# Kernel optimization log

Measured on AMD Instinct MI355X. Metric: run time of the kernel, lower is better.

Reference implementation:

```python
import jax, jax.numpy as jnp
import numpy as np

# Model / shape constants (match init_kwargs and input_specs)
E, H, N, B = 1024, 16, 4096, 4
D = E // H               # head_dim = 64
W_SZ, EXT, C_SZ = 128, 128, 128   # window, ext window, rf chunk
NEG = -1e9


def _linear(x, w, b):
    # torch nn.Linear convention: w is (out, in)
    return x @ w.T + b


def _layernorm(x, g, b, eps=1e-5):
    m = jnp.mean(x, -1, keepdims=True)
    v = jnp.mean((x - m) ** 2, -1, keepdims=True)
    return (x - m) * jax.lax.rsqrt(v + eps) * g + b


def _ext_windows(x, w, ext):
    # x: (b,h,n,d) -> (b,h,g,ext+w,d); window g covers keys [g*w-ext, g*w+w)
    # (front-padded with zeros, same as causal_window_1d_partition + as_strided)
    g = x.shape[2] // w
    xp = jnp.pad(x, ((0, 0), (0, 0), (ext, 0), (0, 0)))
    idx = jnp.arange(g)[:, None] * w + jnp.arange(ext + w)[None, :]
    return xp[:, :, idx]


def setup_inputs() -> dict:
    key = jax.random.key(0)
    ks = jax.random.split(key, 20)
    p = lambda i, shape: jax.random.normal(ks[i], shape, jnp.float32) * 0.02
    return {
        'query': jax.random.normal(ks[0], (N, B, E), jnp.float32),
        'Wq': p(1, (E, E)), 'bq': jnp.zeros((E,), jnp.float32),
        'Wk': p(2, (E, E)), 'bk': jnp.zeros((E,), jnp.float32),
        'Wv': p(3, (E, E)), 'bv': jnp.zeros((E,), jnp.float32),
        'Wo': p(4, (E, E)), 'bo': jnp.zeros((E,), jnp.float32),
        'mu_q_w': p(5, (D, D)), 'mu_q_b': jnp.zeros((D,), jnp.float32),
        'mu_q_g': jnp.ones((D,), jnp.float32), 'mu_q_be': jnp.zeros((D,), jnp.float32),
        'mu_k_w': p(6, (D, D)), 'mu_k_b': jnp.zeros((D,), jnp.float32),
        'mu_k_g': jnp.ones((D,), jnp.float32), 'mu_k_be': jnp.zeros((D,), jnp.float32),
    }


def reference(query, Wq, bq, Wk, bk, Wv, bv, Wo, bo,
              mu_q_w, mu_q_b, mu_q_g, mu_q_be,
              mu_k_w, mu_k_b, mu_k_g, mu_k_be):
    n, b, e = query.shape
    h, d = H, D
    scaling = d ** -0.5

    q = _linear(query, Wq, bq)
    k = _linear(query, Wk, bk)
    v = _linear(query, Wv, bv)
    to_bhnd = lambda t: jnp.transpose(t.reshape(n, b, h, d), (1, 2, 0, 3))
    q, k, v = to_bhnd(q), to_bhnd(k), to_bhnd(v)
    q = q * scaling

    # ---------------- local causal windowed attention scores ----------------
    g = n // W_SZ
    w_q = q.reshape(b, h, g, W_SZ, d)
    w_k = _ext_windows(k, W_SZ, EXT)   # (b,h,g,EXT+W,d)
    w_v = _ext_windows(v, W_SZ, EXT)
    local_dots = jnp.einsum('bhgid,bhgjd->bhgij', w_q, w_k)
    i = jnp.arange(W_SZ)[:, None]
    j = jnp.arange(EXT + W_SZ)[None, :]
    causal_ok = j <= i + EXT                      # key pos <= query pos
    gi = jnp.arange(g)[:, None, None]
    valid = j[None] >= (EXT - gi * W_SZ)          # mask zero-padded front keys
    local_mask = causal_ok[None] & valid          # (g, W, EXT+W)
    local_dots = jnp.where(local_mask[None, None], local_dots, NEG)

    # ------------- random-feature (EVA) chunk-level global branch -------------
    nc = n // C_SZ
    rf_q = q.reshape(b, h, nc, C_SZ, d)
    rf_k = k.reshape(b, h, nc, C_SZ, d)
    rf_v = v.reshape(b, h, nc, C_SZ, d)
    rf_q_bar = _layernorm(_linear(rf_q.mean(-2), mu_q_w, mu_q_b), mu_q_g, mu_q_be)
    rf_k_bar = _layernorm(_linear(rf_k.mean(-2), mu_k_w, mu_k_b), mu_k_g, mu_k_be)
    mu = rf_q_bar + rf_k_bar   # eval mode: weights = mu (no Gaussian noise)

    # prm_projection(rf_k, mu) with normalize=False, then softmax within chunk
    norm = scaling * jnp.sum(rf_k ** 2, -1) / 2.0            # (b,h,nc,p)
    log_proj_k = jnp.einsum('bhcd,bhcpd->bhcp', mu, rf_k) * scaling - norm
    beta = jax.nn.softmax(log_proj_k, -1)
    rfa_chunk = jnp.einsum('bhcp,bhcpd->bhcd', beta, rf_v)   # SNIS chunk values

    rfa_dots = jnp.einsum('bhgid,bhcd->bhgic', w_q, rf_k_bar)
    # chunk c visible to window g iff the whole chunk precedes the window
    chunk_vis = (jnp.arange(nc)[None, :] + 1) * C_SZ <= jnp.arange(g)[:, None] * W_SZ
    rfa_dots = jnp.where(chunk_vis[None, None, :, None, :], rfa_dots, NEG)

    # joint softmax over [local keys | global chunk pseudo-keys]
    attn = jax.nn.softmax(jnp.concatenate([local_dots, rfa_dots], -1), -1)
    la, ga = attn[..., : EXT + W_SZ], attn[..., EXT + W_SZ:]
    out = jnp.einsum('bhgij,bhgjd->bhgid', la, w_v) \
        + jnp.einsum('bhgic,bhcd->bhgid', ga, rfa_chunk)

    out = out.reshape(b, h, n, d)
    out = jnp.transpose(out, (2, 0, 1, 3)).reshape(n, b, e)
    return _linear(out, Wo, bo)
```

## Files before the change

kernel.cpp:

```cpp
#include <hip/hip_runtime.h>
#include <hip/hip_bf16.h>

typedef __hip_bfloat16 bf16;
typedef __attribute__((ext_vector_type(8))) short bf16x8;
typedef __attribute__((ext_vector_type(4))) float f32x4;

#define E_DIM 1024
#define H_DIM 16
#define N_DIM 4096
#define B_DIM 4
#define D_DIM 64
#define G_WIN 32
#define NC 32
#define M_ROWS 16384

__global__ __launch_bounds__(256) void cvt_f32_bf16(
    const float* __restrict__ in, bf16* __restrict__ out)
{
    int i = (blockIdx.x * 256 + threadIdx.x) * 8;
    float4 f0 = *(const float4*)(in + i);
    float4 f1 = *(const float4*)(in + i + 4);
    union { bf16 t[8]; uint4 u; } pk;
    pk.t[0] = (bf16)f0.x; pk.t[1] = (bf16)f0.y; pk.t[2] = (bf16)f0.z; pk.t[3] = (bf16)f0.w;
    pk.t[4] = (bf16)f1.x; pk.t[5] = (bf16)f1.y; pk.t[6] = (bf16)f1.z; pk.t[7] = (bf16)f1.w;
    *(uint4*)(out + i) = pk.u;
}

template<int MODE, bool WB16>
__global__ __launch_bounds__(256) void gemm_mfma(
    const bf16* __restrict__ A, const void* __restrict__ Wp,
    const float* __restrict__ bias, float scale,
    bf16* __restrict__ out_bf, float* __restrict__ out_f)
{
    __shared__ bf16 As[128 * 32];
    __shared__ bf16 Bs[128 * 32];
    int tid  = threadIdx.x;
    int lane = tid & 63;
    int wv   = tid >> 6;
    int wm   = (wv >> 1) * 64;
    int wn   = (wv & 1) * 64;
    int quad = lane >> 4;
    int l16  = lane & 15;

    int nwg = gridDim.x;
    int per = nwg >> 3;
    int logical = (blockIdx.x & 7) * per + (blockIdx.x >> 3);
    int col0 = (logical & 7) * 128;
    int row0 = (logical >> 3) * 128;

    f32x4 acc[4][4] = {};

    for (int k0 = 0; k0 < E_DIM; k0 += 32) {
#pragma unroll
        for (int i = 0; i < 2; i++) {
            int idx = tid + i * 256;
            int r = idx >> 2, c = idx & 3;
            const bf16* g = A + (size_t)(row0 + r) * E_DIM + k0 + c * 8;
            __builtin_amdgcn_global_load_lds(
                (const __attribute__((address_space(1))) void*)g,
                (__attribute__((address_space(3))) void*)(As + idx * 8), 16, 0, 0);
        }
        if constexpr (WB16) {
            const bf16* Wb = (const bf16*)Wp;
#pragma unroll
            for (int i = 0; i < 2; i++) {
                int idx = tid + i * 256;
                int e = idx >> 2, c = idx & 3;
                const bf16* g = Wb + (size_t)(col0 + e) * E_DIM + k0 + c * 8;
                __builtin_amdgcn_global_load_lds(
                    (const __attribute__((address_space(1))) void*)g,
                    (__attribute__((address_space(3))) void*)(Bs + idx * 8), 16, 0, 0);
            }
        } else {
            const float* Wf = (const float*)Wp;
#pragma unroll
            for (int i = 0; i < 2; i++) {
                int idx = tid + i * 256;
                int e = idx >> 2, c = idx & 3;
                const float* wr = Wf + (size_t)(col0 + e) * E_DIM + k0 + c * 8;
                float4 f0 = *(const float4*)wr;
                float4 f1 = *(const float4*)(wr + 4);
                union { bf16 t[8]; uint4 u; } pk;
                pk.t[0] = (bf16)f0.x; pk.t[1] = (bf16)f0.y;
                pk.t[2] = (bf16)f0.z; pk.t[3] = (bf16)f0.w;
                pk.t[4] = (bf16)f1.x; pk.t[5] = (bf16)f1.y;
                pk.t[6] = (bf16)f1.z; pk.t[7] = (bf16)f1.w;
                *(uint4*)(Bs + idx * 8) = pk.u;
            }
        }
        __syncthreads();

        bf16x8 af[4], bfr[4];
#pragma unroll
        for (int t = 0; t < 4; t++) {
            af[t]  = *(const bf16x8*)(As + (wm + t * 16 + l16) * 32 + quad * 8);
            bfr[t] = *(const bf16x8*)(Bs + (wn + t * 16 + l16) * 32 + quad * 8);
        }
#pragma unroll
        for (int mt = 0; mt < 4; mt++)
#pragma unroll
            for (int nt = 0; nt < 4; nt++)
                acc[mt][nt] = __builtin_amdgcn_mfma_f32_16x16x32_bf16(
                    af[mt], bfr[nt], acc[mt][nt], 0, 0, 0);
        __syncthreads();
    }

#pragma unroll
    for (int mt = 0; mt < 4; mt++)
#pragma unroll
        for (int nt = 0; nt < 4; nt++)
#pragma unroll
            for (int rg = 0; rg < 4; rg++) {
                int m = row0 + wm + mt * 16 + quad * 4 + rg;
                int e = col0 + wn + nt * 16 + l16;
                float val = acc[mt][nt][rg];
                if (MODE == 0) {
                    float v2 = (val + bias[e]) * scale;
                    int n = m >> 2, bb = m & 3;
                    int h = e >> 6, d = e & 63;
                    out_bf[((((size_t)bb * H_DIM + h) * N_DIM + n) * D_DIM) + d] = (bf16)v2;
                } else {
                    out_f[(size_t)m * E_DIM + e] = val + bias[e];
                }
            }
}

__global__ __launch_bounds__(128) void chunk_stats(
    const bf16* __restrict__ q_s, const bf16* __restrict__ kbuf, const bf16* __restrict__ vbuf,
    const float* __restrict__ mqw, const float* __restrict__ mqb,
    const float* __restrict__ mqg, const float* __restrict__ mqbe,
    const float* __restrict__ mkw, const float* __restrict__ mkb,
    const float* __restrict__ mkg, const float* __restrict__ mkbe,
    float* __restrict__ rf_k_bar, float* __restrict__ rfa_chunk)
{
    int bid = blockIdx.x;
    int c = bid % NC;
    int bh = bid / NC;
    int tid = threadIdx.x;

    __shared__ float qm[64], km[64], qb_s[64], kb_s[64], mu_s[64], sc[128];
    __shared__ float stats[4];

    size_t base = ((size_t)bh * N_DIM + c * 128) * D_DIM;

    if (tid < 64) {
        float s = 0.f;
        for (int p = 0; p < 128; p++) s += (float)q_s[base + p * 64 + tid];
        qm[tid] = s * (1.0f / 128.0f);
    } else {
        int d = tid - 64;
        float s = 0.f;
        for (int p = 0; p < 128; p++) s += (float)kbuf[base + p * 64 + d];
        km[d] = s * (1.0f / 128.0f);
    }
    __syncthreads();

    if (tid < 64) {
        float t = mqb[tid];
        for (int d2 = 0; d2 < 64; d2++) t += qm[d2] * mqw[tid * 64 + d2];
        qb_s[tid] = t;
    } else {
        int d = tid - 64;
        float t = mkb[d];
        for (int d2 = 0; d2 < 64; d2++) t += km[d2] * mkw[d * 64 + d2];
        kb_s[d] = t;
    }
    __syncthreads();

    if (tid == 0) {
        float m = 0.f;
        for (int d = 0; d < 64; d++) m += qb_s[d];
        m *= (1.0f / 64.0f);
        float vv = 0.f;
        for (int d = 0; d < 64; d++) { float x = qb_s[d] - m; vv += x * x; }
        vv *= (1.0f / 64.0f);
        stats[0] = m; stats[1] = rsqrtf(vv + 1e-5f);
    } else if (tid == 64) {
        float m = 0.f;
        for (int d = 0; d < 64; d++) m += kb_s[d];
        m *= (1.0f / 64.0f);
        float vv = 0.f;
        for (int d = 0; d < 64; d++) { float x = kb_s[d] - m; vv += x * x; }
        vv *= (1.0f / 64.0f);
        stats[2] = m; stats[3] = rsqrtf(vv + 1e-5f);
    }
    __syncthreads();

    if (tid < 64) {
        float qn = (qb_s[tid] - stats[0]) * stats[1] * mqg[tid] + mqbe[tid];
        float kn = (kb_s[tid] - stats[2]) * stats[3] * mkg[tid] + mkbe[tid];
        mu_s[tid] = qn + kn;
        rf_k_bar[(size_t)bh * NC * 64 + c * 64 + tid] = kn;
    }
    __syncthreads();

    {
        float dot = 0.f, ss = 0.f;
        const bf16* kr = kbuf + base + tid * 64;
        for (int d = 0; d < 64; d++) {
            float kv = (float)kr[d];
            dot += mu_s[d] * kv;
            ss += kv * kv;
        }
        sc[tid] = dot * 0.125f - 0.125f * 0.5f * ss;
    }
    __syncthreads();
    if (tid == 0) {
        float m = sc[0];
        for (int p = 1; p < 128; p++) m = fmaxf(m, sc[p]);
        stats[0] = m;
    }
    __syncthreads();
    float e = expf(sc[tid] - stats[0]);
    sc[tid] = e;
    __syncthreads();
    if (tid == 0) {
        float s = 0.f;
        for (int p = 0; p < 128; p++) s += sc[p];
        stats[1] = 1.0f / s;
    }
    __syncthreads();
    sc[tid] *= stats[1];
    __syncthreads();

    if (tid < 64) {
        float acc = 0.f;
        for (int p = 0; p < 128; p++) acc += sc[p] * (float)vbuf[base + p * 64 + tid];
        rfa_chunk[(size_t)bh * NC * 64 + c * 64 + tid] = acc;
    }
}

__global__ __launch_bounds__(512, 4) void attn_kernel(
    const bf16* __restrict__ qin, const bf16* __restrict__ kbuf, const bf16* __restrict__ vbuf,
    const float* __restrict__ rf_k_bar, const float* __restrict__ rfa_chunk,
    bf16* __restrict__ aout)
{
    int bid = blockIdx.x;
    int g = bid & (G_WIN - 1);
    int bh = bid / G_WIN;
    int b = bh >> 4, h = bh & 15;
    int tid = threadIdx.x;
    int lane = tid & 63;
    int wv = tid >> 6;
    int q4 = lane >> 4;
    int l16 = lane & 15;

    __shared__ __align__(16) short Ks[288 * 72];
    __shared__ __align__(16) short Vt[64 * 296];

    size_t kvbase = (size_t)bh * N_DIM * D_DIM;
    int k0g = g * 128 - 128;

#pragma unroll
    for (int i = 0; i < 4; i++) {
        int ci = tid + i * 512;
        int key = ci >> 3, chc = ci & 7;
        int kidx = k0g + key; if (kidx < 0) kidx = 0;
        bf16x8 v = *(const bf16x8*)(kbuf + kvbase + (size_t)kidx * 64 + chc * 8);
        *(bf16x8*)(Ks + key * 72 + chc * 8) = v;
    }
    if (tid < 256) {
        int c = tid >> 3, chc = tid & 7;
        const float* src = rf_k_bar + (size_t)bh * NC * 64 + c * 64 + chc * 8;
        float4 f0 = *(const float4*)src;
        float4 f1 = *(const float4*)(src + 4);
        union { bf16 t[8]; bf16x8 v; } pk;
        pk.t[0] = (bf16)f0.x; pk.t[1] = (bf16)f0.y;
        pk.t[2] = (bf16)f0.z; pk.t[3] = (bf16)f0.w;
        pk.t[4] = (bf16)f1.x; pk.t[5] = (bf16)f1.y;
        pk.t[6] = (bf16)f1.z; pk.t[7] = (bf16)f1.w;
        *(bf16x8*)(Ks + (256 + c) * 72 + chc * 8) = pk.v;
    }
#pragma unroll
    for (int i = 0; i < 4; i++) {
        int ci = tid + i * 512;
        int key = ci & 255, dc = ci >> 8;
        int kidx = k0g + key; if (kidx < 0) kidx = 0;
        union { bf16x8 v; short s[8]; } u;
        u.v = *(const bf16x8*)(vbuf + kvbase + (size_t)kidx * 64 + dc * 8);
#pragma unroll
        for (int jj = 0; jj < 8; jj++)
            Vt[(dc * 8 + jj) * 296 + key] = u.s[jj];
    }
    if (tid < 256) {
        int d = tid >> 2, cg = tid & 3;
        const float* rc = rfa_chunk + (size_t)bh * NC * 64;
#pragma unroll
        for (int jj = 0; jj < 8; jj++) {
            int c = cg * 8 + jj;
            union { bf16 bv; short s; } cv;
            cv.bv = (bf16)rc[(size_t)c * 64 + d];
            Vt[d * 296 + 256 + c] = cv.s;
        }
    }

    bf16x8 aq[2];
    {
        const bf16* qrow = qin + kvbase + (size_t)(g * 128 + wv * 16 + l16) * 64 + q4 * 8;
        aq[0] = *(const bf16x8*)qrow;
        aq[1] = *(const bf16x8*)(qrow + 32);
    }

    __syncthreads();

    f32x4 acc[18] = {};
#pragma unroll
    for (int ct = 0; ct < 18; ct++) {
#pragma unroll
        for (int kc = 0; kc < 2; kc++) {
            bf16x8 bk = *(const bf16x8*)(Ks + (ct * 16 + l16) * 72 + kc * 32 + q4 * 8);
            acc[ct] = __builtin_amdgcn_mfma_f32_16x16x32_bf16(aq[kc], bk, acc[ct], 0, 0, 0);
        }
    }

    __syncthreads();

    float mrow[4] = { -1e30f, -1e30f, -1e30f, -1e30f };
#pragma unroll
    for (int ct = 0; ct < 18; ct++) {
        int j = ct * 16 + l16;
        bool jval = (j < 256) ? (k0g + j >= 0) : ((j - 256) < g);
#pragma unroll
        for (int rg = 0; rg < 4; rg++) {
            int i = wv * 16 + q4 * 4 + rg;
            bool ok = jval && (j >= 256 || j <= i + 128);
            float s = ok ? acc[ct][rg] : -1e9f;
            acc[ct][rg] = s;
            mrow[rg] = fmaxf(mrow[rg], s);
        }
    }
#pragma unroll
    for (int rg = 0; rg < 4; rg++) {
        float v = mrow[rg];
        v = fmaxf(v, __shfl_xor(v, 1));
        v = fmaxf(v, __shfl_xor(v, 2));
        v = fmaxf(v, __shfl_xor(v, 4));
        v = fmaxf(v, __shfl_xor(v, 8));
        mrow[rg] = v;
    }

    float rsum[4] = { 0.f, 0.f, 0.f, 0.f };
#pragma unroll
    for (int ct = 0; ct < 18; ct++)
#pragma unroll
        for (int rg = 0; rg < 4; rg++) {
            float p = __expf(acc[ct][rg] - mrow[rg]);
            acc[ct][rg] = p;
            rsum[rg] += p;
        }
    float rinv[4];
#pragma unroll
    for (int rg = 0; rg < 4; rg++) {
        float v = rsum[rg];
        v += __shfl_xor(v, 1);
        v += __shfl_xor(v, 2);
        v += __shfl_xor(v, 4);
        v += __shfl_xor(v, 8);
        rinv[rg] = 1.0f / v;
    }

    f32x4 accO[4] = {};
    short* pw = Ks + wv * (16 * 40);
#pragma unroll
    for (int cc = 0; cc < 9; cc++) {
#pragma unroll
        for (int half = 0; half < 2; half++) {
            int ct = cc * 2 + half;
#pragma unroll
            for (int rg = 0; rg < 4; rg++) {
                union { bf16 bv; short s; } cv;
                cv.bv = (bf16)acc[ct][rg];
                pw[(q4 * 4 + rg) * 40 + half * 16 + l16] = cv.s;
            }
        }
        bf16x8 ap = *(const bf16x8*)(pw + l16 * 40 + q4 * 8);
#pragma unroll
        for (int dt = 0; dt < 4; dt++) {
            bf16x8 bv = *(const bf16x8*)(Vt + (dt * 16 + l16) * 296 + cc * 32 + q4 * 8);
            accO[dt] = __builtin_amdgcn_mfma_f32_16x16x32_bf16(ap, bv, accO[dt], 0, 0, 0);
        }
    }

    int nbase = g * 128 + wv * 16 + q4 * 4;
#pragma unroll
    for (int dt = 0; dt < 4; dt++)
#pragma unroll
        for (int rg = 0; rg < 4; rg++) {
            float o = accO[dt][rg] * rinv[rg];
            int nn = nbase + rg;
            int d = dt * 16 + l16;
            aout[((size_t)nn * B_DIM + b) * E_DIM + h * 64 + d] = (bf16)o;
        }
}

extern "C" void kernel_launch(void* const* d_in, const int* in_sizes, int n_in,
                              void* d_out, int out_size, void* d_ws, size_t ws_size,
                              hipStream_t stream) {
    const float* query = (const float*)d_in[0];
    const float* Wq   = (const float*)d_in[1];
    const float* bq   = (const float*)d_in[2];
    const float* Wk   = (const float*)d_in[3];
    const float* bk   = (const float*)d_in[4];
    const float* Wv   = (const float*)d_in[5];
    const float* bv   = (const float*)d_in[6];
    const float* Wo   = (const float*)d_in[7];
    const float* bo   = (const float*)d_in[8];
    const float* mqw  = (const float*)d_in[9];
    const float* mqb  = (const float*)d_in[10];
    const float* mqg  = (const float*)d_in[11];
    const float* mqbe = (const float*)d_in[12];
    const float* mkw  = (const float*)d_in[13];
    const float* mkb  = (const float*)d_in[14];
    const float* mkg  = (const float*)d_in[15];
    const float* mkbe = (const float*)d_in[16];

    const size_t SZ = (size_t)B_DIM * H_DIM * N_DIM * D_DIM;
    const size_t STATS = (size_t)B_DIM * H_DIM * NC * D_DIM;

    bf16* kb = (bf16*)d_ws;
    bf16* vb = kb + SZ;
    float* rf_k_bar  = (float*)(vb + SZ);
    float* rfa_chunk = rf_k_bar + STATS;

    size_t base_bytes = 2 * SZ * sizeof(bf16) + 2 * STATS * sizeof(float);
    size_t wmat = (size_t)E_DIM * E_DIM;
    bool wb16   = ws_size >= base_bytes + 4 * wmat * sizeof(bf16);
    bool big_ws = ws_size >= base_bytes + 4 * wmat * sizeof(bf16) + SZ * sizeof(bf16);
    bf16* wq_b = (bf16*)((char*)d_ws + base_bytes);
    bf16* wk_b = wq_b + wmat;
    bf16* wv_b = wk_b + wmat;
    bf16* wo_b = wv_b + wmat;
    bf16* att_ws = wo_b + wmat;

    float* outf = (float*)d_out;
    bf16* qb  = (bf16*)d_out;
    bf16* qbf = qb + SZ;

    dim3 gblk(256);
    int ggrd = (E_DIM / 128) * (M_ROWS / 128);

    cvt_f32_bf16<<<(M_ROWS * E_DIM) / (256 * 8), 256, 0, stream>>>(query, qbf);
    if (wb16) {
        int wblk = (int)(wmat / (256 * 8));
        cvt_f32_bf16<<<wblk, 256, 0, stream>>>(Wq, wq_b);
        cvt_f32_bf16<<<wblk, 256, 0, stream>>>(Wk, wk_b);
        cvt_f32_bf16<<<wblk, 256, 0, stream>>>(Wv, wv_b);
        cvt_f32_bf16<<<wblk, 256, 0, stream>>>(Wo, wo_b);
    }

    if (wb16) {
        gemm_mfma<0, true><<<ggrd, gblk, 0, stream>>>(qbf, wq_b, bq, 0.125f, qb, nullptr);
        gemm_mfma<0, true><<<ggrd, gblk, 0, stream>>>(qbf, wk_b, bk, 1.0f, kb, nullptr);
        gemm_mfma<0, true><<<ggrd, gblk, 0, stream>>>(qbf, wv_b, bv, 1.0f, vb, nullptr);
    } else {
        gemm_mfma<0, false><<<ggrd, gblk, 0, stream>>>(qbf, Wq, bq, 0.125f, qb, nullptr);
        gemm_mfma<0, false><<<ggrd, gblk, 0, stream>>>(qbf, Wk, bk, 1.0f, kb, nullptr);
        gemm_mfma<0, false><<<ggrd, gblk, 0, stream>>>(qbf, Wv, bv, 1.0f, vb, nullptr);
    }

    chunk_stats<<<B_DIM * H_DIM * NC, 128, 0, stream>>>(
        qb, kb, vb, mqw, mqb, mqg, mqbe, mkw, mkb, mkg, mkbe, rf_k_bar, rfa_chunk);

    bf16* attn_dst = big_ws ? att_ws : qbf;
    attn_kernel<<<B_DIM * H_DIM * G_WIN, 512, 0, stream>>>(
        qb, kb, vb, rf_k_bar, rfa_chunk, attn_dst);

    const bf16* gemm_in;
    if (big_ws) {
        gemm_in = att_ws;
    } else {
        (void)hipMemcpyAsync(kb, qbf, SZ * sizeof(bf16), hipMemcpyDeviceToDevice, stream);
        gemm_in = kb;
    }

    if (wb16) {
        gemm_mfma<1, true><<<ggrd, gblk, 0, stream>>>(gemm_in, wo_b, bo, 1.0f, nullptr, outf);
    } else {
        gemm_mfma<1, false><<<ggrd, gblk, 0, stream>>>(gemm_in, Wo, bo, 1.0f, nullptr, outf);
    }
}
```

Before: 432.9 us.

## Compute transposed scores in attention so P stays in registers for PV MFMA

Swaps the MFMA operand order in the windowed attention kernel so each lane holds the scores for one query row. Rows are then reduced with two cross-lane shuffles instead of per-row 4-step shuffles. V columns are stored in a permuted key order so the bf16 probabilities can be packed straight from the accumulators as the PV operand, removing the LDS round trip for P and one __syncthreads. Output is written as packed 4-element stores. The permuted layout must match the MFMA register mapping exactly, or the results will be wrong.

```diff
diff --git a/kernel.cpp b/kernel.cpp
--- a/kernel.cpp
+++ b/kernel.cpp
@@ -13,6 +13,9 @@
 #define G_WIN 32
 #define NC 32
 #define M_ROWS 16384
+
+#define AS1 __attribute__((address_space(1)))
+#define AS3 __attribute__((address_space(3)))
 
 __global__ __launch_bounds__(256) void cvt_f32_bf16(
     const float* __restrict__ in, bf16* __restrict__ out)
@@ -57,8 +60,7 @@
             int r = idx >> 2, c = idx & 3;
             const bf16* g = A + (size_t)(row0 + r) * E_DIM + k0 + c * 8;
             __builtin_amdgcn_global_load_lds(
-                (const __attribute__((address_space(1))) void*)g,
-                (__attribute__((address_space(3))) void*)(As + idx * 8), 16, 0, 0);
+                (const AS1 void*)g, (AS3 void*)(As + idx * 8), 16, 0, 0);
         }
         if constexpr (WB16) {
             const bf16* Wb = (const bf16*)Wp;
@@ -68,8 +70,7 @@
                 int e = idx >> 2, c = idx & 3;
                 const bf16* g = Wb + (size_t)(col0 + e) * E_DIM + k0 + c * 8;
                 __builtin_amdgcn_global_load_lds(
-                    (const __attribute__((address_space(1))) void*)g,
-                    (__attribute__((address_space(3))) void*)(Bs + idx * 8), 16, 0, 0);
+                    (const AS1 void*)g, (AS3 void*)(Bs + idx * 8), 16, 0, 0);
             }
         } else {
             const float* Wf = (const float*)Wp;
@@ -278,9 +279,11 @@
         int kidx = k0g + key; if (kidx < 0) kidx = 0;
         union { bf16x8 v; short s[8]; } u;
         u.v = *(const bf16x8*)(vbuf + kvbase + (size_t)kidx * 64 + dc * 8);
+        int colp = (key & ~31) | (((key >> 2) & 3) << 3)
+                 | (((key >> 4) & 1) << 2) | (key & 3);
 #pragma unroll
         for (int jj = 0; jj < 8; jj++)
-            Vt[(dc * 8 + jj) * 296 + key] = u.s[jj];
+            Vt[(dc * 8 + jj) * 296 + colp] = u.s[jj];
     }
     if (tid < 256) {
         int d = tid >> 2, cg = tid & 3;
@@ -288,17 +291,18 @@
 #pragma unroll
         for (int jj = 0; jj < 8; jj++) {
             int c = cg * 8 + jj;
+            int p = (((c >> 2) & 3) << 3) | (((c >> 4) & 1) << 2) | (c & 3);
             union { bf16 bv; short s; } cv;
             cv.bv = (bf16)rc[(size_t)c * 64 + d];
-            Vt[d * 296 + 256 + c] = cv.s;
-        }
-    }
-
-    bf16x8 aq[2];
+            Vt[d * 296 + 256 + p] = cv.s;
+        }
+    }
+
+    bf16x8 bq0, bq1;
     {
         const bf16* qrow = qin + kvbase + (size_t)(g * 128 + wv * 16 + l16) * 64 + q4 * 8;
-        aq[0] = *(const bf16x8*)qrow;
-        aq[1] = *(const bf16x8*)(qrow + 32);
+        bq0 = *(const bf16x8*)qrow;
+        bq1 = *(const bf16x8*)(qrow + 32);
     }
 
     __syncthreads();
@@ -306,91 +310,68 @@
     f32x4 acc[18] = {};
 #pragma unroll
     for (int ct = 0; ct < 18; ct++) {
-#pragma unroll
-        for (int kc = 0; kc < 2; kc++) {
-            bf16x8 bk = *(const bf16x8*)(Ks + (ct * 16 + l16) * 72 + kc * 32 + q4 * 8);
-            acc[ct] = __builtin_amdgcn_mfma_f32_16x16x32_bf16(aq[kc], bk, acc[ct], 0, 0, 0);
-        }
-    }
-
-    __syncthreads();
-
-    float mrow[4] = { -1e30f, -1e30f, -1e30f, -1e30f };
+        int r = ct * 16 + l16;
+        bf16x8 ak0 = *(const bf16x8*)(Ks + r * 72 + q4 * 8);
+        bf16x8 ak1 = *(const bf16x8*)(Ks + r * 72 + 32 + q4 * 8);
+        acc[ct] = __builtin_amdgcn_mfma_f32_16x16x32_bf16(ak0, bq0, acc[ct], 0, 0, 0);
+        acc[ct] = __builtin_amdgcn_mfma_f32_16x16x32_bf16(ak1, bq1, acc[ct], 0, 0, 0);
+    }
+
+    int qi = wv * 16 + l16;
+    float m = -1e30f;
 #pragma unroll
     for (int ct = 0; ct < 18; ct++) {
-        int j = ct * 16 + l16;
-        bool jval = (j < 256) ? (k0g + j >= 0) : ((j - 256) < g);
+        int jbase = ct * 16 + q4 * 4;
 #pragma unroll
         for (int rg = 0; rg < 4; rg++) {
-            int i = wv * 16 + q4 * 4 + rg;
-            bool ok = jval && (j >= 256 || j <= i + 128);
+            int j = jbase + rg;
+            bool ok = (j < 256) ? (k0g + j >= 0 && j <= qi + 128) : ((j - 256) < g);
             float s = ok ? acc[ct][rg] : -1e9f;
             acc[ct][rg] = s;
-            mrow[rg] = fmaxf(mrow[rg], s);
-        }
-    }
-#pragma unroll
-    for (int rg = 0; rg < 4; rg++) {
-        float v = mrow[rg];
-        v = fmaxf(v, __shfl_xor(v, 1));
-        v = fmaxf(v, __shfl_xor(v, 2));
-        v = fmaxf(v, __shfl_xor(v, 4));
-        v = fmaxf(v, __shfl_xor(v, 8));
-        mrow[rg] = v;
-    }
-
-    float rsum[4] = { 0.f, 0.f, 0.f, 0.f };
+            m = fmaxf(m, s);
+        }
+    }
+    m = fmaxf(m, __shfl_xor(m, 16));
+    m = fmaxf(m, __shfl_xor(m, 32));
+
+    float sum = 0.f;
 #pragma unroll
     for (int ct = 0; ct < 18; ct++)
 #pragma unroll
         for (int rg = 0; rg < 4; rg++) {
-            float p = __expf(acc[ct][rg] - mrow[rg]);
+            float p = __expf(acc[ct][rg] - m);
             acc[ct][rg] = p;
-            rsum[rg] += p;
-        }
-    float rinv[4];
-#pragma unroll
-    for (int rg = 0; rg < 4; rg++) {
-        float v = rsum[rg];
-        v += __shfl_xor(v, 1);
-        v += __shfl_xor(v, 2);
-        v += __shfl_xor(v, 4);
-        v += __shfl_xor(v, 8);
-        rinv[rg] = 1.0f / v;
-    }
+            sum += p;
+        }
+    sum += __shfl_xor(sum, 16);
+    sum += __shfl_xor(sum, 32);
+    float rinv = 1.0f / sum;
 
     f32x4 accO[4] = {};
-    short* pw = Ks + wv * (16 * 40);
 #pragma unroll
     for (int cc = 0; cc < 9; cc++) {
-#pragma unroll
-        for (int half = 0; half < 2; half++) {
-            int ct = cc * 2 + half;
-#pragma unroll
-            for (int rg = 0; rg < 4; rg++) {
-                union { bf16 bv; short s; } cv;
-                cv.bv = (bf16)acc[ct][rg];
-                pw[(q4 * 4 + rg) * 40 + half * 16 + l16] = cv.s;
-            }
-        }
-        bf16x8 ap = *(const bf16x8*)(pw + l16 * 40 + q4 * 8);
+        union { bf16 t[8]; bf16x8 v; } pb;
+#pragma unroll
+        for (int e = 0; e < 4; e++) {
+            pb.t[e]     = (bf16)acc[2 * cc][e];
+            pb.t[4 + e] = (bf16)acc[2 * cc + 1][e];
+        }
 #pragma unroll
         for (int dt = 0; dt < 4; dt++) {
-            bf16x8 bv = *(const bf16x8*)(Vt + (dt * 16 + l16) * 296 + cc * 32 + q4 * 8);
-            accO[dt] = __builtin_amdgcn_mfma_f32_16x16x32_bf16(ap, bv, accO[dt], 0, 0, 0);
-        }
-    }
-
-    int nbase = g * 128 + wv * 16 + q4 * 4;
-#pragma unroll
-    for (int dt = 0; dt < 4; dt++)
-#pragma unroll
-        for (int rg = 0; rg < 4; rg++) {
-            float o = accO[dt][rg] * rinv[rg];
-            int nn = nbase + rg;
-            int d = dt * 16 + l16;
-            aout[((size_t)nn * B_DIM + b) * E_DIM + h * 64 + d] = (bf16)o;
-        }
+            bf16x8 av = *(const bf16x8*)(Vt + (dt * 16 + l16) * 296 + (cc * 4 + q4) * 8);
+            accO[dt] = __builtin_amdgcn_mfma_f32_16x16x32_bf16(av, pb.v, accO[dt], 0, 0, 0);
+        }
+    }
+
+    int nn = g * 128 + wv * 16 + l16;
+    size_t obase = ((size_t)nn * B_DIM + b) * E_DIM + h * 64;
+#pragma unroll
+    for (int dt = 0; dt < 4; dt++) {
+        union { bf16 t[4]; uint2 u; } o;
+#pragma unroll
+        for (int rg = 0; rg < 4; rg++) o.t[rg] = (bf16)(accO[dt][rg] * rinv);
+        *(uint2*)(aout + obase + dt * 16 + q4 * 4) = o.u;
+    }
 }
 
 extern "C" void kernel_launch(void* const* d_in, const int* in_sizes, int n_in,
```

New measurement: 424.1 us. 2.0% less time.
